# Performance work log

Hardware: AMD Instinct MI355X
Metric: run time of the kernel (lower is better)

Reference implementation:

```python
import jax, jax.numpy as jnp
import numpy as np

B, N, C, H, V = 32, 1024, 512, 256, 50  # batch, positions, post_conv_out_channels, hidden_size, out_channels


def setup_inputs() -> dict:
    key = jax.random.key(0)
    ks = jax.random.split(key, 9)
    s = 0.05
    p = lambda k, shape: jax.random.normal(k, shape, jnp.float32) * s
    return dict(
        features=jax.random.normal(ks[0], (B, N, C), jnp.float32),
        w_i2h=p(ks[1], (H, C)),              # input_to_hidden (no bias)
        w_h2h=p(ks[2], (H, H)), b_h2h=jnp.zeros((H,), jnp.float32),
        w_score=p(ks[3], (H,)),              # score Linear(H,1,no bias)
        w_gru_ih=p(ks[4], (3 * H, C + V)), w_gru_hh=p(ks[5], (3 * H, H)),
        b_gru_ih=jnp.zeros((3 * H,), jnp.float32), b_gru_hh=jnp.zeros((3 * H,), jnp.float32),
        w_s1=p(ks[6], (H, H)), b_s1=jnp.zeros((H,), jnp.float32),
        w_s2=p(ks[7], (V, H)), b_s2=jnp.zeros((V,), jnp.float32),
        max_text_length=500,
    )


def reference(features, w_i2h, w_h2h, b_h2h, w_score, w_gru_ih, w_gru_hh,
              b_gru_ih, b_gru_hh, w_s1, b_s1, w_s2, b_s2, max_text_length):
    batch = features.shape[0]
    hid = w_h2h.shape[0]
    vocab = w_s2.shape[0]
    steps = max_text_length + 1
    # input_to_hidden(features) is loop-invariant -> hoist out of the recurrence
    feat_proj = jnp.einsum('bnc,hc->bnh', features, w_i2h)

    def gru_cell(x, h):
        gi = x @ w_gru_ih.T + b_gru_ih
        gh = h @ w_gru_hh.T + b_gru_hh
        i_r, i_z, i_n = jnp.split(gi, 3, axis=-1)
        h_r, h_z, h_n = jnp.split(gh, 3, axis=-1)
        r = jax.nn.sigmoid(i_r + h_r)
        z = jax.nn.sigmoid(i_z + h_z)
        n = jnp.tanh(i_n + r * h_n)
        return (1.0 - z) * n + z * h

    def step(carry, _):
        h, pre = carry
        prev_proj = h @ w_h2h.T + b_h2h                      # [B,H]
        scores = jnp.tanh(feat_proj + prev_proj[:, None, :]) @ w_score  # [B,N]
        alpha = jax.nn.softmax(scores, axis=1)
        ctx = jnp.einsum('bn,bnc->bc', alpha, features)      # [B,C]
        onehot = jax.nn.one_hot(pre, vocab, dtype=features.dtype)
        h_new = gru_cell(jnp.concatenate([ctx, onehot], axis=-1), h)
        struct = (h_new @ w_s1.T + b_s1) @ w_s2.T + b_s2     # structure_generator, [B,V]
        pre_new = jnp.argmax(struct, axis=-1)
        return (h_new, pre_new), struct

    h0 = jnp.zeros((batch, hid), features.dtype)
    pre0 = jnp.zeros((batch,), jnp.int32)
    _, structs = jax.lax.scan(step, (h0, pre0), None, length=steps)  # [T,B,V]
    structs = jnp.transpose(structs, (1, 0, 2))                      # [B,T,V]
    return jax.nn.softmax(structs, axis=-1)
```

## Files before the change

### kernel.cpp

```cpp
#include <hip/hip_runtime.h>
#include <math.h>

#define B_ 32
#define N_ 1024
#define C_ 512
#define H_ 256
#define V_ 50
#define T_ 501
#define CV_ 562
#define G3_ 768
#define CHUNKS_ 32
#define POSB_ 32

typedef float    f32x4 __attribute__((ext_vector_type(4)));
typedef _Float16 f16x4 __attribute__((ext_vector_type(4)));
typedef _Float16 f16x8 __attribute__((ext_vector_type(8)));

__device__ __forceinline__ float fast_rcp(float x) { return __builtin_amdgcn_rcpf(x); }
__device__ __forceinline__ float fast_tanh(float x) {
  float e = __expf(2.0f * x);
  return 1.0f - 2.0f * fast_rcp(e + 1.0f);
}
__device__ __forceinline__ float fast_sigmoid(float x) {
  return fast_rcp(1.0f + __expf(-x));
}

__global__ __launch_bounds__(256) void fp_gemm(const float* __restrict__ A,
                                               const float* __restrict__ W,
                                               _Float16* __restrict__ FPh) {
  __shared__ __align__(16) float As[16][68];
  __shared__ __align__(16) float Ws[16][68];
  const int t = threadIdx.x;
  const int m0 = blockIdx.x * 64;
  const int h0 = blockIdx.y * 64;
  const int lr = t & 63;
  const int kg = t >> 6;
  const int tx = t & 15, ty = t >> 4;
  float acc[4][4] = {};
  for (int k0 = 0; k0 < C_; k0 += 16) {
    float4 av = *(const float4*)&A[(size_t)(m0 + lr) * C_ + k0 + kg * 4];
    float4 wv = *(const float4*)&W[(size_t)(h0 + lr) * C_ + k0 + kg * 4];
    As[kg*4+0][lr] = av.x; As[kg*4+1][lr] = av.y; As[kg*4+2][lr] = av.z; As[kg*4+3][lr] = av.w;
    Ws[kg*4+0][lr] = wv.x; Ws[kg*4+1][lr] = wv.y; Ws[kg*4+2][lr] = wv.z; Ws[kg*4+3][lr] = wv.w;
    __syncthreads();
#pragma unroll
    for (int kk = 0; kk < 16; ++kk) {
      float4 a = *(const float4*)&As[kk][ty * 4];
      float4 w = *(const float4*)&Ws[kk][tx * 4];
      acc[0][0] += a.x*w.x; acc[0][1] += a.x*w.y; acc[0][2] += a.x*w.z; acc[0][3] += a.x*w.w;
      acc[1][0] += a.y*w.x; acc[1][1] += a.y*w.y; acc[1][2] += a.y*w.z; acc[1][3] += a.y*w.w;
      acc[2][0] += a.z*w.x; acc[2][1] += a.z*w.y; acc[2][2] += a.z*w.z; acc[2][3] += a.z*w.w;
      acc[3][0] += a.w*w.x; acc[3][1] += a.w*w.y; acc[3][2] += a.w*w.z; acc[3][3] += a.w*w.w;
    }
    __syncthreads();
  }
#pragma unroll
  for (int i = 0; i < 4; ++i) {
    f16x4 o;
    o.x = (_Float16)acc[i][0]; o.y = (_Float16)acc[i][1];
    o.z = (_Float16)acc[i][2]; o.w = (_Float16)acc[i][3];
    *(f16x4*)&FPh[(size_t)(m0 + ty*4 + i) * H_ + h0 + tx*4] = o;
  }
}

__global__ void feat_to_fp16(const float* __restrict__ src, _Float16* __restrict__ dst,
                             int total4) {
  int i = blockIdx.x * 256 + threadIdx.x;
  if (i >= total4) return;
  f32x4 v = *(const f32x4*)&src[(size_t)i * 4];
  f16x4 o; o.x = (_Float16)v.x; o.y = (_Float16)v.y; o.z = (_Float16)v.z; o.w = (_Float16)v.w;
  *(f16x4*)&dst[(size_t)i * 4] = o;
}

__global__ void transpose_split(const float* __restrict__ src, float* __restrict__ dstA,
                                float* __restrict__ dstB, int rows, int cols, int splitc) {
  int i = blockIdx.x * 256 + threadIdx.x;
  if (i >= rows * cols) return;
  int j = i / cols, c = i - j * cols;
  float v = src[i];
  if (c < splitc) dstA[(size_t)c * rows + j] = v;
  else            dstB[(size_t)(c - splitc) * rows + j] = v;
}

__global__ void init_kernel(const float* __restrict__ b_h2h, float* __restrict__ h,
                            float* __restrict__ pp, int* __restrict__ pre,
                            float* __restrict__ ctx_raw, float* __restrict__ l_total) {
  int i = blockIdx.x * blockDim.x + threadIdx.x;
  if (i < B_ * H_) { h[i] = 0.0f; pp[i] = b_h2h[i & (H_ - 1)]; }
  if (i < B_ * C_) ctx_raw[i] = 0.0f;
  if (i < B_) { pre[i] = 0; l_total[i] = 0.0f; }
}

__global__ __launch_bounds__(256) void k1_attn(
    const _Float16* __restrict__ feath, const _Float16* __restrict__ fph,
    const float* __restrict__ w_score, const float* __restrict__ pp,
    float* __restrict__ ctx_raw, float* __restrict__ l_total) {
  __shared__ __align__(16) float lds_ctx[4 * C_];
  __shared__ float lds_l[4];

  const int t = threadIdx.x;
  const int wv = t >> 6;
  const int lane = t & 63;
  const int b = blockIdx.x >> 5;
  const int chunk = blockIdx.x & (CHUNKS_ - 1);

  float4 ppr = *(const float4*)&pp[b * H_ + lane * 4];
  float4 wsr = *(const float4*)&w_score[lane * 4];
  float aA0 = 0.f, aA1 = 0.f, aA2 = 0.f, aA3 = 0.f;
  float aB0 = 0.f, aB1 = 0.f, aB2 = 0.f, aB3 = 0.f;
  float lacc = 0.f;
  const _Float16* fphb = fph + (size_t)b * N_ * H_;
  const _Float16* fbb  = feath + (size_t)b * N_ * C_;
  const int n0 = chunk * POSB_ + wv * 8;
#pragma unroll 2
  for (int i = 0; i < 8; ++i) {
    const int n = n0 + i;
    f16x4 v = __builtin_nontemporal_load((const f16x4*)&fphb[(size_t)n * H_ + lane * 4]);
    float s = fast_tanh((float)v.x + ppr.x) * wsr.x + fast_tanh((float)v.y + ppr.y) * wsr.y
            + fast_tanh((float)v.z + ppr.z) * wsr.z + fast_tanh((float)v.w + ppr.w) * wsr.w;
#pragma unroll
    for (int off = 32; off > 0; off >>= 1) s += __shfl_xor(s, off);
    float p = __expf(s);
    lacc += p;
    f16x8 f = __builtin_nontemporal_load((const f16x8*)&fbb[(size_t)n * C_ + lane * 8]);
    aA0 += p * (float)f.s0; aA1 += p * (float)f.s1; aA2 += p * (float)f.s2; aA3 += p * (float)f.s3;
    aB0 += p * (float)f.s4; aB1 += p * (float)f.s5; aB2 += p * (float)f.s6; aB3 += p * (float)f.s7;
  }
  {
    float4 o0; o0.x = aA0; o0.y = aA1; o0.z = aA2; o0.w = aA3;
    float4 o1; o1.x = aB0; o1.y = aB1; o1.z = aB2; o1.w = aB3;
    *(float4*)&lds_ctx[wv * C_ + lane * 8] = o0;
    *(float4*)&lds_ctx[wv * C_ + lane * 8 + 4] = o1;
  }
  if (lane == 0) lds_l[wv] = lacc;
  __syncthreads();
  {
    float c0 = lds_ctx[t] + lds_ctx[C_ + t] + lds_ctx[2 * C_ + t] + lds_ctx[3 * C_ + t];
    float c1 = lds_ctx[t + 256] + lds_ctx[C_ + t + 256] + lds_ctx[2 * C_ + t + 256] + lds_ctx[3 * C_ + t + 256];
    unsafeAtomicAdd(&ctx_raw[b * C_ + t], c0);
    unsafeAtomicAdd(&ctx_raw[b * C_ + t + 256], c1);
    if (t == 0) unsafeAtomicAdd(&l_total[b], lds_l[0] + lds_l[1] + lds_l[2] + lds_l[3]);
  }
}

__global__ __launch_bounds__(256) void k2a_gates(
    const float* __restrict__ ctx_raw, const float* __restrict__ h,
    const float* __restrict__ WtA, const float* __restrict__ WtH,
    float* __restrict__ pgi, float* __restrict__ pgh) {
  __shared__ __align__(16) float wlds[64][64];
  __shared__ __align__(16) float clds[32][64];
  const int t = threadIdx.x;
  const int j0 = blockIdx.x * 64;
  const int ks = blockIdx.y;
  const int jl = (t & 31) * 2;
  const int b0 = (t >> 5) * 4;

  float acc[2][4] = {};
#pragma unroll
  for (int kt = 0; kt < 2; ++kt) {
    const int k0 = ks * 128 + kt * 64;
    __syncthreads();
#pragma unroll
    for (int q = 0; q < 4; ++q) {
      int idx = q * 256 + t; int r = idx >> 4, f4 = (idx & 15) * 4;
      *(float4*)&wlds[r][f4] = *(const float4*)&WtA[(size_t)(k0 + r) * G3_ + j0 + f4];
    }
#pragma unroll
    for (int q = 0; q < 2; ++q) {
      int idx = q * 256 + t; int bb = idx >> 4, f4 = (idx & 15) * 4;
      *(float4*)&clds[bb][f4] = *(const float4*)&ctx_raw[(size_t)bb * C_ + k0 + f4];
    }
    __syncthreads();
#pragma unroll 8
    for (int k = 0; k < 64; ++k) {
      float w0 = wlds[k][jl], w1 = wlds[k][jl + 1];
      float x0 = clds[b0][k], x1 = clds[b0 + 1][k], x2 = clds[b0 + 2][k], x3 = clds[b0 + 3][k];
      acc[0][0] += w0 * x0; acc[0][1] += w0 * x1; acc[0][2] += w0 * x2; acc[0][3] += w0 * x3;
      acc[1][0] += w1 * x0; acc[1][1] += w1 * x1; acc[1][2] += w1 * x2; acc[1][3] += w1 * x3;
    }
  }
#pragma unroll
  for (int i = 0; i < 2; ++i)
#pragma unroll
    for (int q = 0; q < 4; ++q)
      pgi[((size_t)ks * B_ + b0 + q) * G3_ + j0 + jl + i] = acc[i][q];

  float acb[2][4] = {};
  {
    const int k0 = ks * 64;
    __syncthreads();
#pragma unroll
    for (int q = 0; q < 4; ++q) {
      int idx = q * 256 + t; int r = idx >> 4, f4 = (idx & 15) * 4;
      *(float4*)&wlds[r][f4] = *(const float4*)&WtH[(size_t)(k0 + r) * G3_ + j0 + f4];
    }
#pragma unroll
    for (int q = 0; q < 2; ++q) {
      int idx = q * 256 + t; int bb = idx >> 4, f4 = (idx & 15) * 4;
      *(float4*)&clds[bb][f4] = *(const float4*)&h[(size_t)bb * H_ + k0 + f4];
    }
    __syncthreads();
#pragma unroll 8
    for (int k = 0; k < 64; ++k) {
      float w0 = wlds[k][jl], w1 = wlds[k][jl + 1];
      float x0 = clds[b0][k], x1 = clds[b0 + 1][k], x2 = clds[b0 + 2][k], x3 = clds[b0 + 3][k];
      acb[0][0] += w0 * x0; acb[0][1] += w0 * x1; acb[0][2] += w0 * x2; acb[0][3] += w0 * x3;
      acb[1][0] += w1 * x0; acb[1][1] += w1 * x1; acb[1][2] += w1 * x2; acb[1][3] += w1 * x3;
    }
  }
#pragma unroll
  for (int i = 0; i < 2; ++i)
#pragma unroll
    for (int q = 0; q < 4; ++q)
      pgh[((size_t)ks * B_ + b0 + q) * G3_ + j0 + jl + i] = acb[i][q];
}

__global__ __launch_bounds__(512) void k2b_tail(
    int tstep,
    const float* __restrict__ pgi, const float* __restrict__ pgh,
    const float* __restrict__ l_total_c,
    const float* __restrict__ WtO,
    const float* __restrict__ b_gru_ih, const float* __restrict__ b_gru_hh,
    const float* __restrict__ Wt_s1, const float* __restrict__ b_s1,
    const float* __restrict__ Wt_h2h, const float* __restrict__ b_h2h,
    const float* __restrict__ w_s2, const float* __restrict__ b_s2,
    float* __restrict__ h, float* __restrict__ pp, int* __restrict__ pre,
    float* __restrict__ ctx_raw, float* __restrict__ l_total,
    float* __restrict__ out) {
  __shared__ __align__(16) float shn[H_];
  __shared__ __align__(16) float ss1[H_];
  __shared__ float sst[64];
  const int b = blockIdx.x;
  const int t = threadIdx.x;
  const int prev = pre[b];
  const float invl = 1.0f / l_total_c[b];

  if (t < H_) {
    float gi0 = 0.f, gi1 = 0.f, gi2 = 0.f, gh0 = 0.f, gh1 = 0.f, gh2 = 0.f;
#pragma unroll
    for (int ks = 0; ks < 4; ++ks) {
      const float* pg = pgi + ((size_t)ks * B_ + b) * G3_;
      const float* ph = pgh + ((size_t)ks * B_ + b) * G3_;
      gi0 += pg[t]; gi1 += pg[t + 256]; gi2 += pg[t + 512];
      gh0 += ph[t]; gh1 += ph[t + 256]; gh2 += ph[t + 512];
    }
    const float* wo = WtO + (size_t)prev * G3_;
    gi0 = gi0 * invl + b_gru_ih[t]       + wo[t];
    gi1 = gi1 * invl + b_gru_ih[t + 256] + wo[t + 256];
    gi2 = gi2 * invl + b_gru_ih[t + 512] + wo[t + 512];
    gh0 += b_gru_hh[t]; gh1 += b_gru_hh[t + 256]; gh2 += b_gru_hh[t + 512];
    const float h_old = h[b * H_ + t];
    const float r = fast_sigmoid(gi0 + gh0);
    const float z = fast_sigmoid(gi1 + gh1);
    const float nn = fast_tanh(gi2 + r * gh2);
    const float hnew = (1.0f - z) * nn + z * h_old;
    h[b * H_ + t] = hnew;
    shn[t] = hnew;
  }
  ctx_raw[b * C_ + t] = 0.0f;
  if (t == 0) l_total[b] = 0.0f;
  __syncthreads();

  if (t < H_) {
    float acc = b_s1[t];
    const float* w1 = Wt_s1 + t;
#pragma unroll 8
    for (int c = 0; c < H_; ++c) acc += w1[(size_t)c * H_] * shn[c];
    ss1[t] = acc;
  } else if (t < 2 * H_) {
    const int tt = t - H_;
    float acc = b_h2h[tt];
    const float* wh2 = Wt_h2h + tt;
#pragma unroll 8
    for (int c = 0; c < H_; ++c) acc += wh2[(size_t)c * H_] * shn[c];
    pp[b * H_ + tt] = acc;
  }
  __syncthreads();

  const int wv = t >> 6, lane = t & 63;
  for (int v = wv; v < V_; v += 8) {
    float4 wr = *(const float4*)&w_s2[(size_t)v * H_ + lane * 4];
    float4 sv = *(const float4*)&ss1[lane * 4];
    float acc = wr.x * sv.x + wr.y * sv.y + wr.z * sv.z + wr.w * sv.w;
#pragma unroll
    for (int off = 32; off > 0; off >>= 1) acc += __shfl_xor(acc, off);
    if (lane == 0) sst[v] = acc + b_s2[v];
  }
  __syncthreads();

  if (t < 64) {
    float val = (lane < V_) ? sst[lane] : -INFINITY;
    float m = val;
#pragma unroll
    for (int off = 32; off > 0; off >>= 1) m = fmaxf(m, __shfl_xor(m, off));
    unsigned long long msk = __ballot(val == m);
    int amax = __ffsll(msk) - 1;
    float e = (lane < V_) ? __expf(val - m) : 0.0f;
    float ssum = e;
#pragma unroll
    for (int off = 32; off > 0; off >>= 1) ssum += __shfl_xor(ssum, off);
    if (lane < V_) out[((size_t)b * T_ + tstep) * V_ + lane] = e / ssum;
    if (lane == 0) pre[b] = amax;
  }
}

extern "C" void kernel_launch(void* const* d_in, const int* in_sizes, int n_in,
                              void* d_out, int out_size, void* d_ws, size_t ws_size,
                              hipStream_t stream) {
  (void)in_sizes; (void)n_in; (void)out_size; (void)ws_size;
  const float* feat     = (const float*)d_in[0];
  const float* w_i2h    = (const float*)d_in[1];
  const float* w_h2h    = (const float*)d_in[2];
  const float* b_h2h    = (const float*)d_in[3];
  const float* w_score  = (const float*)d_in[4];
  const float* w_gru_ih = (const float*)d_in[5];
  const float* w_gru_hh = (const float*)d_in[6];
  const float* b_gru_ih = (const float*)d_in[7];
  const float* b_gru_hh = (const float*)d_in[8];
  const float* w_s1     = (const float*)d_in[9];
  const float* b_s1     = (const float*)d_in[10];
  const float* w_s2     = (const float*)d_in[11];
  const float* b_s2     = (const float*)d_in[12];
  float* out = (float*)d_out;

  char* ws = (char*)d_ws;
  size_t off = 0;
  auto alloc = [&](size_t bytes) { void* p = ws + off; off += (bytes + 255) & ~(size_t)255; return p; };
  _Float16* fph   = (_Float16*)alloc((size_t)B_ * N_ * H_ * 2);
  _Float16* feath = (_Float16*)alloc((size_t)B_ * N_ * C_ * 2);
  float* ctx_raw  = (float*)alloc((size_t)B_ * C_ * 4);
  float* l_total  = (float*)alloc((size_t)B_ * 4);
  float* pgi      = (float*)alloc((size_t)4 * B_ * G3_ * 4);
  float* pgh      = (float*)alloc((size_t)4 * B_ * G3_ * 4);
  float* WtA      = (float*)alloc((size_t)C_ * G3_ * 4);
  float* WtO      = (float*)alloc((size_t)V_ * G3_ * 4);
  float* WtH      = (float*)alloc((size_t)H_ * G3_ * 4);
  float* Wt_s1    = (float*)alloc((size_t)H_ * H_ * 4);
  float* Wt_h2h   = (float*)alloc((size_t)H_ * H_ * 4);
  float* h        = (float*)alloc((size_t)B_ * H_ * 4);
  float* pp       = (float*)alloc((size_t)B_ * H_ * 4);
  int*   pre      = (int*)alloc((size_t)B_ * 4);

  init_kernel<<<64, 256, 0, stream>>>(b_h2h, h, pp, pre, ctx_raw, l_total);
  fp_gemm<<<dim3((B_ * N_) / 64, H_ / 64), 256, 0, stream>>>(feat, w_i2h, fph);
  feat_to_fp16<<<(B_ * N_ * C_ / 4 + 255) / 256, 256, 0, stream>>>(feat, feath, B_ * N_ * C_ / 4);
  transpose_split<<<(G3_ * CV_ + 255) / 256, 256, 0, stream>>>(w_gru_ih, WtA, WtO, G3_, CV_, C_);
  transpose_split<<<(G3_ * H_ + 255) / 256, 256, 0, stream>>>(w_gru_hh, WtH, WtH, G3_, H_, H_);
  transpose_split<<<(H_ * H_ + 255) / 256, 256, 0, stream>>>(w_s1, Wt_s1, Wt_s1, H_, H_, H_);
  transpose_split<<<(H_ * H_ + 255) / 256, 256, 0, stream>>>(w_h2h, Wt_h2h, Wt_h2h, H_, H_, H_);

  for (int tstep = 0; tstep < T_; ++tstep) {
    k1_attn<<<B_ * CHUNKS_, 256, 0, stream>>>(feath, fph, w_score, pp, ctx_raw, l_total);
    k2a_gates<<<dim3(12, 4), 256, 0, stream>>>(ctx_raw, h, WtA, WtH, pgi, pgh);
    k2b_tail<<<B_, 512, 0, stream>>>(tstep, pgi, pgh, l_total, WtO,
                                     b_gru_ih, b_gru_hh, Wt_s1, b_s1, Wt_h2h, b_h2h,
                                     w_s2, b_s2, h, pp, pre, ctx_raw, l_total, out);
  }
}
```

Baseline: 17.58 ms.

## Fuse per-step attention, gate GEMM and tail into one kernel with ticket counters

```diff
diff --git a/kernel.cpp b/kernel.cpp
--- a/kernel.cpp
+++ b/kernel.cpp
@@ -9,8 +9,11 @@
 #define T_ 501
 #define CV_ 562
 #define G3_ 768
-#define CHUNKS_ 32
-#define POSB_ 32
+#define ATTN_BLKS 512
+#define GATE_BLKS 48
+#define TAIL_BLKS 32
+#define WORK_BLKS 80
+#define CHUNKS_ 16
 
 typedef float    f32x4 __attribute__((ext_vector_type(4)));
 typedef _Float16 f16x4 __attribute__((ext_vector_type(4)));
@@ -23,6 +26,12 @@
 }
 __device__ __forceinline__ float fast_sigmoid(float x) {
   return fast_rcp(1.0f + __expf(-x));
+}
+__device__ __forceinline__ float aload(const float* p) {
+  return __hip_atomic_load(p, __ATOMIC_RELAXED, __HIP_MEMORY_SCOPE_AGENT);
+}
+__device__ __forceinline__ int aloadi(const int* p) {
+  return __hip_atomic_load(p, __ATOMIC_RELAXED, __HIP_MEMORY_SCOPE_AGENT);
 }
 
 __global__ __launch_bounds__(256) void fp_gemm(const float* __restrict__ A,
@@ -84,223 +93,246 @@
 
 __global__ void init_kernel(const float* __restrict__ b_h2h, float* __restrict__ h,
                             float* __restrict__ pp, int* __restrict__ pre,
-                            float* __restrict__ ctx_raw, float* __restrict__ l_total) {
+                            float* __restrict__ ctx_raw, float* __restrict__ l_total,
+                            float* __restrict__ gi_raw, float* __restrict__ gh_raw,
+                            int* __restrict__ cnt) {
   int i = blockIdx.x * blockDim.x + threadIdx.x;
   if (i < B_ * H_) { h[i] = 0.0f; pp[i] = b_h2h[i & (H_ - 1)]; }
   if (i < B_ * C_) ctx_raw[i] = 0.0f;
+  if (i < B_ * G3_) { gi_raw[i] = 0.0f; gh_raw[i] = 0.0f; }
+  if (i < T_ * 2) cnt[i] = 0;
   if (i < B_) { pre[i] = 0; l_total[i] = 0.0f; }
 }
 
-__global__ __launch_bounds__(256) void k1_attn(
+__global__ __launch_bounds__(256) void step_fused(
+    int tstep,
     const _Float16* __restrict__ feath, const _Float16* __restrict__ fph,
-    const float* __restrict__ w_score, const float* __restrict__ pp,
-    float* __restrict__ ctx_raw, float* __restrict__ l_total) {
-  __shared__ __align__(16) float lds_ctx[4 * C_];
-  __shared__ float lds_l[4];
-
-  const int t = threadIdx.x;
-  const int wv = t >> 6;
-  const int lane = t & 63;
-  const int b = blockIdx.x >> 5;
-  const int chunk = blockIdx.x & (CHUNKS_ - 1);
-
-  float4 ppr = *(const float4*)&pp[b * H_ + lane * 4];
-  float4 wsr = *(const float4*)&w_score[lane * 4];
-  float aA0 = 0.f, aA1 = 0.f, aA2 = 0.f, aA3 = 0.f;
-  float aB0 = 0.f, aB1 = 0.f, aB2 = 0.f, aB3 = 0.f;
-  float lacc = 0.f;
-  const _Float16* fphb = fph + (size_t)b * N_ * H_;
-  const _Float16* fbb  = feath + (size_t)b * N_ * C_;
-  const int n0 = chunk * POSB_ + wv * 8;
-#pragma unroll 2
-  for (int i = 0; i < 8; ++i) {
-    const int n = n0 + i;
-    f16x4 v = __builtin_nontemporal_load((const f16x4*)&fphb[(size_t)n * H_ + lane * 4]);
-    float s = fast_tanh((float)v.x + ppr.x) * wsr.x + fast_tanh((float)v.y + ppr.y) * wsr.y
-            + fast_tanh((float)v.z + ppr.z) * wsr.z + fast_tanh((float)v.w + ppr.w) * wsr.w;
-#pragma unroll
-    for (int off = 32; off > 0; off >>= 1) s += __shfl_xor(s, off);
-    float p = __expf(s);
-    lacc += p;
-    f16x8 f = __builtin_nontemporal_load((const f16x8*)&fbb[(size_t)n * C_ + lane * 8]);
-    aA0 += p * (float)f.s0; aA1 += p * (float)f.s1; aA2 += p * (float)f.s2; aA3 += p * (float)f.s3;
-    aB0 += p * (float)f.s4; aB1 += p * (float)f.s5; aB2 += p * (float)f.s6; aB3 += p * (float)f.s7;
-  }
-  {
-    float4 o0; o0.x = aA0; o0.y = aA1; o0.z = aA2; o0.w = aA3;
-    float4 o1; o1.x = aB0; o1.y = aB1; o1.z = aB2; o1.w = aB3;
-    *(float4*)&lds_ctx[wv * C_ + lane * 8] = o0;
-    *(float4*)&lds_ctx[wv * C_ + lane * 8 + 4] = o1;
-  }
-  if (lane == 0) lds_l[wv] = lacc;
-  __syncthreads();
-  {
-    float c0 = lds_ctx[t] + lds_ctx[C_ + t] + lds_ctx[2 * C_ + t] + lds_ctx[3 * C_ + t];
-    float c1 = lds_ctx[t + 256] + lds_ctx[C_ + t + 256] + lds_ctx[2 * C_ + t + 256] + lds_ctx[3 * C_ + t + 256];
-    unsafeAtomicAdd(&ctx_raw[b * C_ + t], c0);
-    unsafeAtomicAdd(&ctx_raw[b * C_ + t + 256], c1);
-    if (t == 0) unsafeAtomicAdd(&l_total[b], lds_l[0] + lds_l[1] + lds_l[2] + lds_l[3]);
-  }
-}
-
-__global__ __launch_bounds__(256) void k2a_gates(
-    const float* __restrict__ ctx_raw, const float* __restrict__ h,
+    const float* __restrict__ w_score, float* __restrict__ pp,
+    float* __restrict__ ctx_raw, float* __restrict__ l_total,
+    float* __restrict__ gi_raw, float* __restrict__ gh_raw,
     const float* __restrict__ WtA, const float* __restrict__ WtH,
-    float* __restrict__ pgi, float* __restrict__ pgh) {
-  __shared__ __align__(16) float wlds[64][64];
-  __shared__ __align__(16) float clds[32][64];
-  const int t = threadIdx.x;
-  const int j0 = blockIdx.x * 64;
-  const int ks = blockIdx.y;
-  const int jl = (t & 31) * 2;
-  const int b0 = (t >> 5) * 4;
-
-  float acc[2][4] = {};
-#pragma unroll
-  for (int kt = 0; kt < 2; ++kt) {
-    const int k0 = ks * 128 + kt * 64;
-    __syncthreads();
-#pragma unroll
-    for (int q = 0; q < 4; ++q) {
-      int idx = q * 256 + t; int r = idx >> 4, f4 = (idx & 15) * 4;
-      *(float4*)&wlds[r][f4] = *(const float4*)&WtA[(size_t)(k0 + r) * G3_ + j0 + f4];
-    }
-#pragma unroll
-    for (int q = 0; q < 2; ++q) {
-      int idx = q * 256 + t; int bb = idx >> 4, f4 = (idx & 15) * 4;
-      *(float4*)&clds[bb][f4] = *(const float4*)&ctx_raw[(size_t)bb * C_ + k0 + f4];
-    }
-    __syncthreads();
-#pragma unroll 8
-    for (int k = 0; k < 64; ++k) {
-      float w0 = wlds[k][jl], w1 = wlds[k][jl + 1];
-      float x0 = clds[b0][k], x1 = clds[b0 + 1][k], x2 = clds[b0 + 2][k], x3 = clds[b0 + 3][k];
-      acc[0][0] += w0 * x0; acc[0][1] += w0 * x1; acc[0][2] += w0 * x2; acc[0][3] += w0 * x3;
-      acc[1][0] += w1 * x0; acc[1][1] += w1 * x1; acc[1][2] += w1 * x2; acc[1][3] += w1 * x3;
-    }
-  }
-#pragma unroll
-  for (int i = 0; i < 2; ++i)
-#pragma unroll
-    for (int q = 0; q < 4; ++q)
-      pgi[((size_t)ks * B_ + b0 + q) * G3_ + j0 + jl + i] = acc[i][q];
-
-  float acb[2][4] = {};
-  {
-    const int k0 = ks * 64;
-    __syncthreads();
-#pragma unroll
-    for (int q = 0; q < 4; ++q) {
-      int idx = q * 256 + t; int r = idx >> 4, f4 = (idx & 15) * 4;
-      *(float4*)&wlds[r][f4] = *(const float4*)&WtH[(size_t)(k0 + r) * G3_ + j0 + f4];
-    }
-#pragma unroll
-    for (int q = 0; q < 2; ++q) {
-      int idx = q * 256 + t; int bb = idx >> 4, f4 = (idx & 15) * 4;
-      *(float4*)&clds[bb][f4] = *(const float4*)&h[(size_t)bb * H_ + k0 + f4];
-    }
-    __syncthreads();
-#pragma unroll 8
-    for (int k = 0; k < 64; ++k) {
-      float w0 = wlds[k][jl], w1 = wlds[k][jl + 1];
-      float x0 = clds[b0][k], x1 = clds[b0 + 1][k], x2 = clds[b0 + 2][k], x3 = clds[b0 + 3][k];
-      acb[0][0] += w0 * x0; acb[0][1] += w0 * x1; acb[0][2] += w0 * x2; acb[0][3] += w0 * x3;
-      acb[1][0] += w1 * x0; acb[1][1] += w1 * x1; acb[1][2] += w1 * x2; acb[1][3] += w1 * x3;
-    }
-  }
-#pragma unroll
-  for (int i = 0; i < 2; ++i)
-#pragma unroll
-    for (int q = 0; q < 4; ++q)
-      pgh[((size_t)ks * B_ + b0 + q) * G3_ + j0 + jl + i] = acb[i][q];
-}
-
-__global__ __launch_bounds__(512) void k2b_tail(
-    int tstep,
-    const float* __restrict__ pgi, const float* __restrict__ pgh,
-    const float* __restrict__ l_total_c,
     const float* __restrict__ WtO,
     const float* __restrict__ b_gru_ih, const float* __restrict__ b_gru_hh,
     const float* __restrict__ Wt_s1, const float* __restrict__ b_s1,
     const float* __restrict__ Wt_h2h, const float* __restrict__ b_h2h,
     const float* __restrict__ w_s2, const float* __restrict__ b_s2,
-    float* __restrict__ h, float* __restrict__ pp, int* __restrict__ pre,
-    float* __restrict__ ctx_raw, float* __restrict__ l_total,
-    float* __restrict__ out) {
-  __shared__ __align__(16) float shn[H_];
-  __shared__ __align__(16) float ss1[H_];
-  __shared__ float sst[64];
-  const int b = blockIdx.x;
+    float* __restrict__ h, int* __restrict__ pre,
+    int* __restrict__ cnt, float* __restrict__ out) {
+  __shared__ __align__(16) float smem[6144];
+  __shared__ float lds_l[4];
+  __shared__ int sticket;
+
   const int t = threadIdx.x;
-  const int prev = pre[b];
-  const float invl = 1.0f / l_total_c[b];
-
-  if (t < H_) {
-    float gi0 = 0.f, gi1 = 0.f, gi2 = 0.f, gh0 = 0.f, gh1 = 0.f, gh2 = 0.f;
-#pragma unroll
-    for (int ks = 0; ks < 4; ++ks) {
-      const float* pg = pgi + ((size_t)ks * B_ + b) * G3_;
-      const float* ph = pgh + ((size_t)ks * B_ + b) * G3_;
-      gi0 += pg[t]; gi1 += pg[t + 256]; gi2 += pg[t + 512];
-      gh0 += ph[t]; gh1 += ph[t + 256]; gh2 += ph[t + 512];
-    }
+  const int wv = t >> 6;
+  const int lane = t & 63;
+  int* c1 = &cnt[tstep * 2];
+  int* c2 = &cnt[tstep * 2 + 1];
+
+  {
+    const int b = blockIdx.x >> 4;
+    const int chunk = blockIdx.x & (CHUNKS_ - 1);
+    float4 ppr = *(const float4*)&pp[b * H_ + lane * 4];
+    float4 wsr = *(const float4*)&w_score[lane * 4];
+    float aA0 = 0.f, aA1 = 0.f, aA2 = 0.f, aA3 = 0.f;
+    float aB0 = 0.f, aB1 = 0.f, aB2 = 0.f, aB3 = 0.f;
+    float lacc = 0.f;
+    const _Float16* fphb = fph + (size_t)b * N_ * H_;
+    const _Float16* fbb  = feath + (size_t)b * N_ * C_;
+    const int n0 = chunk * 64 + wv * 16;
+#pragma unroll 2
+    for (int i = 0; i < 16; ++i) {
+      const int n = n0 + i;
+      f16x4 v = __builtin_nontemporal_load((const f16x4*)&fphb[(size_t)n * H_ + lane * 4]);
+      float s = fast_tanh((float)v.x + ppr.x) * wsr.x + fast_tanh((float)v.y + ppr.y) * wsr.y
+              + fast_tanh((float)v.z + ppr.z) * wsr.z + fast_tanh((float)v.w + ppr.w) * wsr.w;
+#pragma unroll
+      for (int off = 32; off > 0; off >>= 1) s += __shfl_xor(s, off);
+      float p = __expf(s);
+      lacc += p;
+      f16x8 f = __builtin_nontemporal_load((const f16x8*)&fbb[(size_t)n * C_ + lane * 8]);
+      aA0 += p * (float)f.s0; aA1 += p * (float)f.s1; aA2 += p * (float)f.s2; aA3 += p * (float)f.s3;
+      aB0 += p * (float)f.s4; aB1 += p * (float)f.s5; aB2 += p * (float)f.s6; aB3 += p * (float)f.s7;
+    }
+    {
+      float4 o0; o0.x = aA0; o0.y = aA1; o0.z = aA2; o0.w = aA3;
+      float4 o1; o1.x = aB0; o1.y = aB1; o1.z = aB2; o1.w = aB3;
+      *(float4*)&smem[wv * C_ + lane * 8] = o0;
+      *(float4*)&smem[wv * C_ + lane * 8 + 4] = o1;
+    }
+    if (lane == 0) lds_l[wv] = lacc;
+    __syncthreads();
+    {
+      float c0v = smem[t] + smem[C_ + t] + smem[2 * C_ + t] + smem[3 * C_ + t];
+      float c1v = smem[t + 256] + smem[C_ + t + 256] + smem[2 * C_ + t + 256] + smem[3 * C_ + t + 256];
+      unsafeAtomicAdd(&ctx_raw[b * C_ + t], c0v);
+      unsafeAtomicAdd(&ctx_raw[b * C_ + t + 256], c1v);
+      if (t == 0) unsafeAtomicAdd(&l_total[b], lds_l[0] + lds_l[1] + lds_l[2] + lds_l[3]);
+    }
+  }
+  asm volatile("s_waitcnt vmcnt(0)" ::: "memory");
+  __syncthreads();
+  if (t == 0) sticket = atomicAdd(c1, 1);
+  __syncthreads();
+  const int ticket = sticket;
+  if (ticket < ATTN_BLKS - WORK_BLKS) return;
+
+  if (t == 0) {
+    while (aloadi(c1) < ATTN_BLKS) __builtin_amdgcn_s_sleep(2);
+  }
+  __syncthreads();
+
+  if (ticket < ATTN_BLKS - TAIL_BLKS) {
+    const int rid = ticket - (ATTN_BLKS - WORK_BLKS);
+    const int jg = rid % 12, ks = rid / 12;
+    const int j0 = jg * 64;
+    const int jl = (t & 31) * 2;
+    const int b0 = (t >> 5) * 4;
+    float* wlds = smem;
+    float* clds = smem + 4096;
+
+    float acc[2][4] = {};
+#pragma unroll
+    for (int kt = 0; kt < 2; ++kt) {
+      const int k0 = ks * 128 + kt * 64;
+      __syncthreads();
+#pragma unroll
+      for (int q = 0; q < 4; ++q) {
+        int idx = q * 256 + t; int r = idx >> 4, f4 = (idx & 15) * 4;
+        *(float4*)&wlds[r * 64 + f4] = *(const float4*)&WtA[(size_t)(k0 + r) * G3_ + j0 + f4];
+      }
+#pragma unroll
+      for (int q = 0; q < 8; ++q) {
+        int idx = q * 256 + t; int bb = idx >> 6, k = idx & 63;
+        clds[bb * 64 + k] = aload(&ctx_raw[bb * C_ + k0 + k]);
+      }
+      __syncthreads();
+#pragma unroll 8
+      for (int k = 0; k < 64; ++k) {
+        float w0 = wlds[k * 64 + jl], w1 = wlds[k * 64 + jl + 1];
+        float x0 = clds[b0 * 64 + k], x1 = clds[(b0 + 1) * 64 + k];
+        float x2 = clds[(b0 + 2) * 64 + k], x3 = clds[(b0 + 3) * 64 + k];
+        acc[0][0] += w0 * x0; acc[0][1] += w0 * x1; acc[0][2] += w0 * x2; acc[0][3] += w0 * x3;
+        acc[1][0] += w1 * x0; acc[1][1] += w1 * x1; acc[1][2] += w1 * x2; acc[1][3] += w1 * x3;
+      }
+    }
+#pragma unroll
+    for (int i = 0; i < 2; ++i)
+#pragma unroll
+      for (int q = 0; q < 4; ++q)
+        unsafeAtomicAdd(&gi_raw[(size_t)(b0 + q) * G3_ + j0 + jl + i], acc[i][q]);
+
+    float acb[2][4] = {};
+    {
+      const int k0 = ks * 64;
+      __syncthreads();
+#pragma unroll
+      for (int q = 0; q < 4; ++q) {
+        int idx = q * 256 + t; int r = idx >> 4, f4 = (idx & 15) * 4;
+        *(float4*)&wlds[r * 64 + f4] = *(const float4*)&WtH[(size_t)(k0 + r) * G3_ + j0 + f4];
+      }
+#pragma unroll
+      for (int q = 0; q < 8; ++q) {
+        int idx = q * 256 + t; int bb = idx >> 6, k = idx & 63;
+        clds[bb * 64 + k] = h[bb * H_ + k0 + k];
+      }
+      __syncthreads();
+#pragma unroll 8
+      for (int k = 0; k < 64; ++k) {
+        float w0 = wlds[k * 64 + jl], w1 = wlds[k * 64 + jl + 1];
+        float x0 = clds[b0 * 64 + k], x1 = clds[(b0 + 1) * 64 + k];
+        float x2 = clds[(b0 + 2) * 64 + k], x3 = clds[(b0 + 3) * 64 + k];
+        acb[0][0] += w0 * x0; acb[0][1] += w0 * x1; acb[0][2] += w0 * x2; acb[0][3] += w0 * x3;
+        acb[1][0] += w1 * x0; acb[1][1] += w1 * x1; acb[1][2] += w1 * x2; acb[1][3] += w1 * x3;
+      }
+    }
+#pragma unroll
+    for (int i = 0; i < 2; ++i)
+#pragma unroll
+      for (int q = 0; q < 4; ++q)
+        unsafeAtomicAdd(&gh_raw[(size_t)(b0 + q) * G3_ + j0 + jl + i], acb[i][q]);
+
+    asm volatile("s_waitcnt vmcnt(0)" ::: "memory");
+    __syncthreads();
+    if (t == 0) atomicAdd(c2, 1);
+    return;
+  }
+
+  if (t == 0) {
+    while (aloadi(c2) < GATE_BLKS) __builtin_amdgcn_s_sleep(2);
+  }
+  __syncthreads();
+  {
+    const int b = ticket - (ATTN_BLKS - TAIL_BLKS);
+    float* shn = smem;
+    float* ss1 = smem + 256;
+    float* sst = smem + 512;
+    const int prev = pre[b];
+    const float invl = 1.0f / aload(&l_total[b]);
+    float gi0 = aload(&gi_raw[b * G3_ + t]);
+    float gi1 = aload(&gi_raw[b * G3_ + t + 256]);
+    float gi2 = aload(&gi_raw[b * G3_ + t + 512]);
+    float gh0 = aload(&gh_raw[b * G3_ + t]);
+    float gh1 = aload(&gh_raw[b * G3_ + t + 256]);
+    float gh2 = aload(&gh_raw[b * G3_ + t + 512]);
+    const float h_old = h[b * H_ + t];
+    __syncthreads();
+    gi_raw[b * G3_ + t] = 0.0f; gi_raw[b * G3_ + t + 256] = 0.0f; gi_raw[b * G3_ + t + 512] = 0.0f;
+    gh_raw[b * G3_ + t] = 0.0f; gh_raw[b * G3_ + t + 256] = 0.0f; gh_raw[b * G3_ + t + 512] = 0.0f;
+    ctx_raw[b * C_ + t] = 0.0f; ctx_raw[b * C_ + t + 256] = 0.0f;
+    if (t == 0) l_total[b] = 0.0f;
+
     const float* wo = WtO + (size_t)prev * G3_;
     gi0 = gi0 * invl + b_gru_ih[t]       + wo[t];
     gi1 = gi1 * invl + b_gru_ih[t + 256] + wo[t + 256];
     gi2 = gi2 * invl + b_gru_ih[t + 512] + wo[t + 512];
     gh0 += b_gru_hh[t]; gh1 += b_gru_hh[t + 256]; gh2 += b_gru_hh[t + 512];
-    const float h_old = h[b * H_ + t];
     const float r = fast_sigmoid(gi0 + gh0);
     const float z = fast_sigmoid(gi1 + gh1);
     const float nn = fast_tanh(gi2 + r * gh2);
     const float hnew = (1.0f - z) * nn + z * h_old;
     h[b * H_ + t] = hnew;
     shn[t] = hnew;
-  }
-  ctx_raw[b * C_ + t] = 0.0f;
-  if (t == 0) l_total[b] = 0.0f;
-  __syncthreads();
-
-  if (t < H_) {
-    float acc = b_s1[t];
-    const float* w1 = Wt_s1 + t;
+    __syncthreads();
+
+    {
+      float a1 = b_s1[t], a2 = b_h2h[t];
+      const float* w1 = Wt_s1 + t;
+      const float* w2 = Wt_h2h + t;
 #pragma unroll 8
-    for (int c = 0; c < H_; ++c) acc += w1[(size_t)c * H_] * shn[c];
-    ss1[t] = acc;
-  } else if (t < 2 * H_) {
-    const int tt = t - H_;
-    float acc = b_h2h[tt];
-    const float* wh2 = Wt_h2h + tt;
-#pragma unroll 8
-    for (int c = 0; c < H_; ++c) acc += wh2[(size_t)c * H_] * shn[c];
-    pp[b * H_ + tt] = acc;
-  }
-  __syncthreads();
-
-  const int wv = t >> 6, lane = t & 63;
-  for (int v = wv; v < V_; v += 8) {
-    float4 wr = *(const float4*)&w_s2[(size_t)v * H_ + lane * 4];
-    float4 sv = *(const float4*)&ss1[lane * 4];
-    float acc = wr.x * sv.x + wr.y * sv.y + wr.z * sv.z + wr.w * sv.w;
-#pragma unroll
-    for (int off = 32; off > 0; off >>= 1) acc += __shfl_xor(acc, off);
-    if (lane == 0) sst[v] = acc + b_s2[v];
-  }
-  __syncthreads();
-
-  if (t < 64) {
-    float val = (lane < V_) ? sst[lane] : -INFINITY;
-    float m = val;
-#pragma unroll
-    for (int off = 32; off > 0; off >>= 1) m = fmaxf(m, __shfl_xor(m, off));
-    unsigned long long msk = __ballot(val == m);
-    int amax = __ffsll(msk) - 1;
-    float e = (lane < V_) ? __expf(val - m) : 0.0f;
-    float ssum = e;
-#pragma unroll
-    for (int off = 32; off > 0; off >>= 1) ssum += __shfl_xor(ssum, off);
-    if (lane < V_) out[((size_t)b * T_ + tstep) * V_ + lane] = e / ssum;
-    if (lane == 0) pre[b] = amax;
+      for (int c = 0; c < H_; ++c) {
+        float v = shn[c];
+        a1 += w1[(size_t)c * H_] * v;
+        a2 += w2[(size_t)c * H_] * v;
+      }
+      ss1[t] = a1;
+      pp[b * H_ + t] = a2;
+    }
+    __syncthreads();
+
+    for (int v = wv; v < V_; v += 4) {
+      float4 wr = *(const float4*)&w_s2[(size_t)v * H_ + lane * 4];
+      float4 sv = *(const float4*)&ss1[lane * 4];
+      float acc = wr.x * sv.x + wr.y * sv.y + wr.z * sv.z + wr.w * sv.w;
+#pragma unroll
+      for (int off = 32; off > 0; off >>= 1) acc += __shfl_xor(acc, off);
+      if (lane == 0) sst[v] = acc + b_s2[v];
+    }
+    __syncthreads();
+
+    if (t < 64) {
+      float val = (lane < V_) ? sst[lane] : -INFINITY;
+      float m = val;
+#pragma unroll
+      for (int off = 32; off > 0; off >>= 1) m = fmaxf(m, __shfl_xor(m, off));
+      unsigned long long msk = __ballot(val == m);
+      int amax = __ffsll(msk) - 1;
+      float e = (lane < V_) ? __expf(val - m) : 0.0f;
+      float ssum = e;
+#pragma unroll
+      for (int off = 32; off > 0; off >>= 1) ssum += __shfl_xor(ssum, off);
+      if (lane < V_) out[((size_t)b * T_ + tstep) * V_ + lane] = e / ssum;
+      if (lane == 0) pre[b] = amax;
+    }
   }
 }
 
@@ -330,8 +362,8 @@
   _Float16* feath = (_Float16*)alloc((size_t)B_ * N_ * C_ * 2);
   float* ctx_raw  = (float*)alloc((size_t)B_ * C_ * 4);
   float* l_total  = (float*)alloc((size_t)B_ * 4);
-  float* pgi      = (float*)alloc((size_t)4 * B_ * G3_ * 4);
-  float* pgh      = (float*)alloc((size_t)4 * B_ * G3_ * 4);
+  float* gi_raw   = (float*)alloc((size_t)B_ * G3_ * 4);
+  float* gh_raw   = (float*)alloc((size_t)B_ * G3_ * 4);
   float* WtA      = (float*)alloc((size_t)C_ * G3_ * 4);
   float* WtO      = (float*)alloc((size_t)V_ * G3_ * 4);
   float* WtH      = (float*)alloc((size_t)H_ * G3_ * 4);
@@ -340,8 +372,9 @@
   float* h        = (float*)alloc((size_t)B_ * H_ * 4);
   float* pp       = (float*)alloc((size_t)B_ * H_ * 4);
   int*   pre      = (int*)alloc((size_t)B_ * 4);
-
-  init_kernel<<<64, 256, 0, stream>>>(b_h2h, h, pp, pre, ctx_raw, l_total);
+  int*   cnt      = (int*)alloc((size_t)T_ * 2 * 4);
+
+  init_kernel<<<128, 256, 0, stream>>>(b_h2h, h, pp, pre, ctx_raw, l_total, gi_raw, gh_raw, cnt);
   fp_gemm<<<dim3((B_ * N_) / 64, H_ / 64), 256, 0, stream>>>(feat, w_i2h, fph);
   feat_to_fp16<<<(B_ * N_ * C_ / 4 + 255) / 256, 256, 0, stream>>>(feat, feath, B_ * N_ * C_ / 4);
   transpose_split<<<(G3_ * CV_ + 255) / 256, 256, 0, stream>>>(w_gru_ih, WtA, WtO, G3_, CV_, C_);
@@ -350,10 +383,9 @@
   transpose_split<<<(H_ * H_ + 255) / 256, 256, 0, stream>>>(w_h2h, Wt_h2h, Wt_h2h, H_, H_, H_);
 
   for (int tstep = 0; tstep < T_; ++tstep) {
-    k1_attn<<<B_ * CHUNKS_, 256, 0, stream>>>(feath, fph, w_score, pp, ctx_raw, l_total);
-    k2a_gates<<<dim3(12, 4), 256, 0, stream>>>(ctx_raw, h, WtA, WtH, pgi, pgh);
-    k2b_tail<<<B_, 512, 0, stream>>>(tstep, pgi, pgh, l_total, WtO,
-                                     b_gru_ih, b_gru_hh, Wt_s1, b_s1, Wt_h2h, b_h2h,
-                                     w_s2, b_s2, h, pp, pre, ctx_raw, l_total, out);
-  }
-}
+    step_fused<<<ATTN_BLKS, 256, 0, stream>>>(
+        tstep, feath, fph, w_score, pp, ctx_raw, l_total, gi_raw, gh_raw,
+        WtA, WtH, WtO, b_gru_ih, b_gru_hh, Wt_s1, b_s1, Wt_h2h, b_h2h,
+        w_s2, b_s2, h, pre, cnt, out);
+  }
+}
```

Measured after the change: 22.77 ms. 29.6% more time.
